# Kernel tuning notes

Measured on AMD Instinct MI355X. Metric: run time of the kernel, lower is better.

## Reference

```python
import jax, jax.numpy as jnp
import numpy as np

KERNEL = 5  # hardcoded moving-average kernel size in the model
PAD = (KERNEL - 1) // 2


def setup_inputs() -> dict:
    key = jax.random.key(0)
    k1, k2, k3, k4, k5 = jax.random.split(key, 5)
    b, seq_len, pred_len, c = 64, 336, 720, 33 * 54
    x = jax.random.normal(k1, (b, seq_len, c), dtype=jnp.float32)
    W_seasonal = jax.random.normal(k2, (pred_len, seq_len), dtype=jnp.float32) * 0.02
    b_seasonal = jax.random.normal(k3, (pred_len,), dtype=jnp.float32) * 0.02
    W_trend = jax.random.normal(k4, (pred_len, seq_len), dtype=jnp.float32) * 0.02
    b_trend = jax.random.normal(k5, (pred_len,), dtype=jnp.float32) * 0.02
    return {"x": x, "W_seasonal": W_seasonal, "b_seasonal": b_seasonal,
            "W_trend": W_trend, "b_trend": b_trend}


def _moving_avg(x):
    # x: [b, t, c]; replicate-pad the time axis then k-window mean (stride 1)
    xp = jnp.pad(x, ((0, 0), (PAD, PAD), (0, 0)), mode="edge")
    cs = jnp.cumsum(xp, axis=1)
    cs = jnp.concatenate([jnp.zeros_like(cs[:, :1]), cs], axis=1)
    return (cs[:, KERNEL:] - cs[:, :-KERNEL]) / KERNEL  # [b, t, c]


def reference(x, W_seasonal, b_seasonal, W_trend, b_trend):
    # All 33 chunks use the same weights, so the per-chunk loop is equivalent
    # to processing the full 1782-channel tensor at once.
    trend = _moving_avg(x)            # [b, t, c]
    seasonal = x - trend              # [b, t, c]
    # torch Linear over the time axis: y[b,p,c] = sum_t x[b,t,c] * W[p,t] + bias[p]
    out = (jnp.einsum("btc,pt->bpc", seasonal, W_seasonal) + b_seasonal[None, :, None]
           + jnp.einsum("btc,pt->bpc", trend, W_trend) + b_trend[None, :, None])
    return jnp.maximum(out, 0.0)      # torch.clip(min=0)
```

## Files before the change

kernel.cpp:

```cpp
#include <hip/hip_runtime.h>
#include <hip/hip_bf16.h>
#include <stdint.h>

#define T_SEQ 336
#define NKT   11
#define P_LEN 720
#define NM16  48
#define C_LEN 1782
#define NB    64
#define CTILE 112
#define NCT   16
#define BPITCH 360

typedef __attribute__((ext_vector_type(4))) float f32x4;
typedef __attribute__((ext_vector_type(8))) short s16x8;

__device__ __forceinline__ unsigned short f2bf(float f) {
  unsigned int u = __builtin_bit_cast(unsigned int, f);
  u += 0x7FFFu + ((u >> 16) & 1u);
  return (unsigned short)(u >> 16);
}

__global__ __launch_bounds__(64) void prep_w(
    const float* __restrict__ Ws, const float* __restrict__ bs,
    const float* __restrict__ Wt, const float* __restrict__ bt,
    unsigned short* __restrict__ apack, float* __restrict__ bias) {
  const int p   = blockIdx.x;
  const int tid = threadIdx.x;
  if (tid < NKT * 4) {
    const int kt = tid >> 2;
    const int lg = tid & 3;
    const float* wsr = Ws + (size_t)p * T_SEQ;
    const float* wtr = Wt + (size_t)p * T_SEQ;
    union { s16x8 v; unsigned short u[8]; } pk;
#pragma unroll
    for (int j = 0; j < 8; ++j) {
      const int k = kt * 32 + lg * 8 + j;
      float val = 0.f;
      if (p < P_LEN && k < T_SEQ) {
        float d;
        if (k == 0) {
          d = 3.f*(wtr[0]-wsr[0]) + 2.f*(wtr[1]-wsr[1]) + (wtr[2]-wsr[2]);
        } else if (k == T_SEQ-1) {
          d = 3.f*(wtr[T_SEQ-1]-wsr[T_SEQ-1]) + 2.f*(wtr[T_SEQ-2]-wsr[T_SEQ-2])
              + (wtr[T_SEQ-3]-wsr[T_SEQ-3]);
        } else {
          int lo = (k-2 < 0) ? 0 : k-2;
          int hi = (k+2 > T_SEQ-1) ? T_SEQ-1 : k+2;
          d = 0.f;
          for (int t = lo; t <= hi; ++t) d += wtr[t]-wsr[t];
        }
        val = wsr[k] + 0.2f*d;
      }
      pk.u[j] = f2bf(val);
    }
    const int m16 = p >> 4;
    const int l16 = p & 15;
    *(s16x8*)&apack[(size_t)(((m16*NKT + kt) * 64) + lg*16 + l16) * 8] = pk.v;
  }
  if (tid == 0 && p < P_LEN) bias[p] = bs[p] + bt[p];
}

__global__ __launch_bounds__(512, 4) void gemm_kernel(
    const float* __restrict__ x, const unsigned short* __restrict__ apack,
    const float* __restrict__ bias, float* __restrict__ out) {
  __shared__ __align__(16) unsigned short Bp[CTILE * BPITCH];

  const int bid = blockIdx.x;
  const int xcd = bid & 7;
  const int ct  = (xcd << 1) | ((bid >> 3) & 1);
  const int b   = bid >> 4;
  const int c0  = ct * CTILE;

  const int tid  = threadIdx.x;
  const int lane = tid & 63;
  const int wid  = tid >> 6;
  const int l16  = lane & 15;
  const int lg   = lane >> 4;

  const float* xb = x + (size_t)b * T_SEQ * C_LEN;
  const s16x8* ap = (const s16x8*)apack;

  for (int i = tid; i < 42 * 56; i += 512) {
    const int cp = i % 56;
    const int kg = i / 56;
    int c = c0 + cp * 2; if (c > C_LEN - 2) c = C_LEN - 2;
    float2 v[8];
#pragma unroll
    for (int j = 0; j < 8; ++j)
      v[j] = *(const float2*)(xb + (size_t)(kg * 8 + j) * C_LEN + c);
    union { s16x8 vv; uint32_t dw[4]; } pa, pb;
#pragma unroll
    for (int h = 0; h < 4; ++h) {
      uint32_t ra, rb;
      asm("v_cvt_pk_bf16_f32 %0, %1, %2" : "=v"(ra) : "v"(v[2*h].x), "v"(v[2*h+1].x));
      asm("v_cvt_pk_bf16_f32 %0, %1, %2" : "=v"(rb) : "v"(v[2*h].y), "v"(v[2*h+1].y));
      pa.dw[h] = ra; pb.dw[h] = rb;
    }
    *(s16x8*)&Bp[(cp * 2)     * BPITCH + kg * 8] = pa.vv;
    *(s16x8*)&Bp[(cp * 2 + 1) * BPITCH + kg * 8] = pb.vv;
  }
  {
    const s16x8 z = {};
    for (int i = tid; i < CTILE * 3; i += 512)
      *(s16x8*)&Bp[(i / 3) * BPITCH + T_SEQ + (i % 3) * 8] = z;
  }
  __syncthreads();

  const size_t ob = (size_t)b * P_LEN * C_LEN;

#pragma unroll 1
  for (int mp = 0; mp < 3; ++mp) {
    const int m16a = mp * 16 + wid * 2;
    float bv[2][4];
#pragma unroll
    for (int m = 0; m < 2; ++m) {
      const int pb0 = (m16a + m) * 16 + lg * 4;
#pragma unroll
      for (int r = 0; r < 4; ++r)
        bv[m][r] = (pb0 + r < P_LEN) ? bias[pb0 + r] : 0.f;
    }

    f32x4 acc[2][7] = {};
    s16x8 afc0 = ap[(size_t)((m16a)     * NKT) * 64 + lane];
    s16x8 afc1 = ap[(size_t)((m16a + 1) * NKT) * 64 + lane];

#pragma unroll
    for (int kt = 0; kt < NKT; ++kt) {
      s16x8 afn0, afn1;
      if (kt + 1 < NKT) {
        afn0 = ap[(size_t)((m16a)     * NKT + kt + 1) * 64 + lane];
        afn1 = ap[(size_t)((m16a + 1) * NKT + kt + 1) * 64 + lane];
      }
      s16x8 bf[7];
#pragma unroll
      for (int n = 0; n < 7; ++n)
        bf[n] = *(const s16x8*)&Bp[(n * 16 + l16) * BPITCH + kt * 32 + lg * 8];
      __builtin_amdgcn_sched_barrier(0);
#pragma unroll
      for (int n = 0; n < 7; ++n) {
        acc[0][n] = __builtin_amdgcn_mfma_f32_16x16x32_bf16(
            afc0, bf[n], acc[0][n], 0, 0, 0);
        acc[1][n] = __builtin_amdgcn_mfma_f32_16x16x32_bf16(
            afc1, bf[n], acc[1][n], 0, 0, 0);
      }
      if (kt + 1 < NKT) { afc0 = afn0; afc1 = afn1; }
    }

#pragma unroll
    for (int m = 0; m < 2; ++m) {
      const int m16 = m16a + m;
      if (m16 < 45) {
        const int pb0 = m16 * 16 + lg * 4;
#pragma unroll
        for (int n = 0; n < 7; ++n) {
          const int cc = c0 + n * 16 + l16;
          if (cc < C_LEN) {
#pragma unroll
            for (int r = 0; r < 4; ++r) {
              float vv = acc[m][n][r] + bv[m][r];
              out[ob + (size_t)(pb0 + r) * C_LEN + cc] = fmaxf(vv, 0.f);
            }
          }
        }
      }
    }
  }
}

extern "C" void kernel_launch(void* const* d_in, const int* in_sizes, int n_in,
                              void* d_out, int out_size, void* d_ws, size_t ws_size,
                              hipStream_t stream) {
  (void)in_sizes; (void)n_in; (void)out_size; (void)ws_size;
  const float* x  = (const float*)d_in[0];
  const float* Ws = (const float*)d_in[1];
  const float* bs = (const float*)d_in[2];
  const float* Wt = (const float*)d_in[3];
  const float* bt = (const float*)d_in[4];
  float* out = (float*)d_out;

  unsigned short* apack = (unsigned short*)d_ws;
  float* biasp = (float*)((char*)d_ws + (size_t)NM16 * NKT * 1024);

  prep_w<<<dim3(768), dim3(64), 0, stream>>>(Ws, bs, Wt, bt, apack, biasp);
  gemm_kernel<<<dim3(NB * NCT), dim3(512), 0, stream>>>(x, apack, biasp, out);
}
```

Before: 195.9 us.

## Transpose MFMA output for vectorized row stores and retile channels to 96

Swaps the MFMA operands so each lane holds four consecutive channels of a single output row. The epilogue can then write 16-byte vector stores with a per-row bias instead of scalar strided stores. The channel tile shrinks from 112 to 96 (19 tiles), which lowers per-block LDS use. The block-to-tile mapping is re-swizzled across the 8 XCDs. Rows of 1782 floats are not 16-byte aligned for odd rows, so some vector stores are misaligned, and the narrower tile adds padding waste.

```diff
diff --git a/kernel.cpp b/kernel.cpp
--- a/kernel.cpp
+++ b/kernel.cpp
@@ -8,8 +8,9 @@
 #define NM16  48
 #define C_LEN 1782
 #define NB    64
-#define CTILE 112
-#define NCT   16
+#define CTILE 96
+#define NCT   19
+#define NFR   6
 #define BPITCH 360
 
 typedef __attribute__((ext_vector_type(4))) float f32x4;
@@ -67,9 +68,9 @@
   __shared__ __align__(16) unsigned short Bp[CTILE * BPITCH];
 
   const int bid = blockIdx.x;
-  const int xcd = bid & 7;
-  const int ct  = (xcd << 1) | ((bid >> 3) & 1);
-  const int b   = bid >> 4;
+  const int swz = (bid & 7) * 152 + (bid >> 3);
+  const int b   = swz / NCT;
+  const int ct  = swz % NCT;
   const int c0  = ct * CTILE;
 
   const int tid  = threadIdx.x;
@@ -81,9 +82,9 @@
   const float* xb = x + (size_t)b * T_SEQ * C_LEN;
   const s16x8* ap = (const s16x8*)apack;
 
-  for (int i = tid; i < 42 * 56; i += 512) {
-    const int cp = i % 56;
-    const int kg = i / 56;
+  for (int i = tid; i < 42 * 48; i += 512) {
+    const int cp = i % 48;
+    const int kg = i / 48;
     int c = c0 + cp * 2; if (c > C_LEN - 2) c = C_LEN - 2;
     float2 v[8];
 #pragma unroll
@@ -112,16 +113,8 @@
 #pragma unroll 1
   for (int mp = 0; mp < 3; ++mp) {
     const int m16a = mp * 16 + wid * 2;
-    float bv[2][4];
-#pragma unroll
-    for (int m = 0; m < 2; ++m) {
-      const int pb0 = (m16a + m) * 16 + lg * 4;
-#pragma unroll
-      for (int r = 0; r < 4; ++r)
-        bv[m][r] = (pb0 + r < P_LEN) ? bias[pb0 + r] : 0.f;
-    }
 
-    f32x4 acc[2][7] = {};
+    f32x4 acc[2][NFR] = {};
     s16x8 afc0 = ap[(size_t)((m16a)     * NKT) * 64 + lane];
     s16x8 afc1 = ap[(size_t)((m16a + 1) * NKT) * 64 + lane];
 
@@ -132,17 +125,17 @@
         afn0 = ap[(size_t)((m16a)     * NKT + kt + 1) * 64 + lane];
         afn1 = ap[(size_t)((m16a + 1) * NKT + kt + 1) * 64 + lane];
       }
-      s16x8 bf[7];
+      s16x8 bf[NFR];
 #pragma unroll
-      for (int n = 0; n < 7; ++n)
+      for (int n = 0; n < NFR; ++n)
         bf[n] = *(const s16x8*)&Bp[(n * 16 + l16) * BPITCH + kt * 32 + lg * 8];
       __builtin_amdgcn_sched_barrier(0);
 #pragma unroll
-      for (int n = 0; n < 7; ++n) {
+      for (int n = 0; n < NFR; ++n) {
         acc[0][n] = __builtin_amdgcn_mfma_f32_16x16x32_bf16(
-            afc0, bf[n], acc[0][n], 0, 0, 0);
+            bf[n], afc0, acc[0][n], 0, 0, 0);
         acc[1][n] = __builtin_amdgcn_mfma_f32_16x16x32_bf16(
-            afc1, bf[n], acc[1][n], 0, 0, 0);
+            bf[n], afc1, acc[1][n], 0, 0, 0);
       }
       if (kt + 1 < NKT) { afc0 = afn0; afc1 = afn1; }
     }
@@ -151,16 +144,20 @@
     for (int m = 0; m < 2; ++m) {
       const int m16 = m16a + m;
       if (m16 < 45) {
-        const int pb0 = m16 * 16 + lg * 4;
+        const float bvm = bias[m16 * 16 + l16];
+        float* rowp = out + ob + (size_t)(m16 * 16 + l16) * C_LEN;
 #pragma unroll
-        for (int n = 0; n < 7; ++n) {
-          const int cc = c0 + n * 16 + l16;
-          if (cc < C_LEN) {
+        for (int n = 0; n < NFR; ++n) {
+          const int cb = c0 + n * 16 + lg * 4;
+          f32x4 v;
 #pragma unroll
-            for (int r = 0; r < 4; ++r) {
-              float vv = acc[m][n][r] + bv[m][r];
-              out[ob + (size_t)(pb0 + r) * C_LEN + cc] = fmaxf(vv, 0.f);
-            }
+          for (int r = 0; r < 4; ++r) v[r] = fmaxf(acc[m][n][r] + bvm, 0.f);
+          if (cb + 3 < C_LEN) {
+            *(f32x4*)(rowp + cb) = v;
+          } else {
+#pragma unroll
+            for (int r = 0; r < 4; ++r)
+              if (cb + r < C_LEN) rowp[cb + r] = v[r];
           }
         }
       }
```

After: 172.5 us. 12.0% less time.
